# Kernel tuning notes

Measured on AMD Instinct MI355X. Metric: run time of the kernel, lower is better.

Reference implementation:

```python
import jax, jax.numpy as jnp
import numpy as np

N, E = 50000, 640000
DIN, DH, DOUT = 128, 256, 128


def _glorot(k, i, o):
    return jax.random.normal(k, (i, o), jnp.float32) / np.sqrt(i)


def setup_inputs() -> dict:
    key = jax.random.key(0)
    ks = jax.random.split(key, 12)
    return {
        "x": jax.random.normal(ks[0], (N, DIN), jnp.float32),
        "edge_index": jax.random.randint(ks[1], (2, E), 0, N, dtype=jnp.int32),
        # SAGEConv 1: in -> hidden (lin_l on aggregated w/ bias, lin_r on root)
        "W1l": _glorot(ks[2], DIN, DH), "b1l": jnp.zeros((DH,), jnp.float32), "W1r": _glorot(ks[3], DIN, DH),
        "g1": jnp.ones((DH,), jnp.float32), "be1": jnp.zeros((DH,), jnp.float32),
        # skip projection (in != hidden)
        "Wsk": _glorot(ks[4], DIN, DH), "bsk": jnp.zeros((DH,), jnp.float32),
        # SAGEConv 2: hidden -> hidden
        "W2l": _glorot(ks[5], DH, DH), "b2l": jnp.zeros((DH,), jnp.float32), "W2r": _glorot(ks[6], DH, DH),
        "g2": jnp.ones((DH,), jnp.float32), "be2": jnp.zeros((DH,), jnp.float32),
        # SAGEConv 3: hidden -> out
        "W3l": _glorot(ks[7], DH, DOUT), "b3l": jnp.zeros((DOUT,), jnp.float32), "W3r": _glorot(ks[8], DH, DOUT),
    }


def _sage_conv(x, src, dst, Wl, bl, Wr, n):
    # mean aggregation of source features into destination nodes
    msg = x[src]                                                 # [E, d]
    agg = jax.ops.segment_sum(msg, dst, num_segments=n)          # [N, d]
    cnt = jax.ops.segment_sum(jnp.ones((src.shape[0],), x.dtype), dst, num_segments=n)
    agg = agg / jnp.maximum(cnt, 1.0)[:, None]
    return agg @ Wl + bl + x @ Wr


def _layernorm(x, g, b):
    mu = jnp.mean(x, axis=-1, keepdims=True)
    var = jnp.mean((x - mu) ** 2, axis=-1, keepdims=True)
    return (x - mu) * jax.lax.rsqrt(var + 1e-5) * g + b


def reference(x, edge_index, W1l, b1l, W1r, g1, be1, Wsk, bsk,
              W2l, b2l, W2r, g2, be2, W3l, b3l, W3r):
    src, dst = edge_index[0], edge_index[1]
    n = x.shape[0]
    # layer 0: conv -> LN -> relu -> (dropout p=0, eval) -> skip via projection
    h = _sage_conv(x, src, dst, W1l, b1l, W1r, n)
    h = jax.nn.relu(_layernorm(h, g1, be1))
    h = h + (x @ Wsk + bsk)
    # layer 1: conv -> LN -> relu -> residual add (shapes match)
    h2 = _sage_conv(h, src, dst, W2l, b2l, W2r, n)
    h2 = jax.nn.relu(_layernorm(h2, g2, be2)) + h
    # final conv (no norm/act)
    return _sage_conv(h2, src, dst, W3l, b3l, W3r, n)
```

## Files before the change

### kernel.cpp

```cpp
#include <hip/hip_runtime.h>


typedef float floatx4 __attribute__((ext_vector_type(4)));
typedef float floatx2 __attribute__((ext_vector_type(2)));
typedef short bf16x8 __attribute__((ext_vector_type(8)));

__device__ inline unsigned short f2bf(float f) {
    unsigned u = __float_as_uint(f);
    unsigned r = (u + 0x7fffu + ((u >> 16) & 1u)) >> 16;
    return (unsigned short)r;
}
__device__ inline float bf2f_lo(unsigned v) { return __uint_as_float(v << 16); }
__device__ inline float bf2f_hi(unsigned v) { return __uint_as_float(v & 0xffff0000u); }

__device__ inline void gl_lds16(const void* g, void* l) {
    __builtin_amdgcn_global_load_lds((const __attribute__((address_space(1))) unsigned int*)g,
                                     (__attribute__((address_space(3))) unsigned int*)l,
                                     16, 0, 0);
}

__global__ void hist_kernel(const int* __restrict__ dst, int* __restrict__ cnt, int E) {
    int i = blockIdx.x * blockDim.x + threadIdx.x;
    if (i < E) atomicAdd(&cnt[dst[i]], 1);
}

#define SCAN_CHUNK 2048

__global__ __launch_bounds__(256) void scan_blocksums(const int* __restrict__ cnt,
                                                      int* __restrict__ bsum, int N) {
    __shared__ int sh[256];
    int t = threadIdx.x;
    int base = blockIdx.x * SCAN_CHUNK + t * 8;
    int s = 0;
#pragma unroll
    for (int i = 0; i < 8; i++) {
        int idx = base + i;
        if (idx < N) s += cnt[idx];
    }
    sh[t] = s;
    __syncthreads();
    for (int off = 1; off < 256; off <<= 1) {
        int v = (t >= off) ? sh[t - off] : 0;
        __syncthreads();
        sh[t] += v;
        __syncthreads();
    }
    if (t == 255) bsum[blockIdx.x] = sh[255];
}

__global__ __launch_bounds__(256) void scan_bsums(const int* __restrict__ bsum,
                                                  int* __restrict__ boff, int NB,
                                                  int* __restrict__ rowptr, int N, int E) {
    __shared__ int sh[256];
    int t = threadIdx.x;
    int v = (t < NB) ? bsum[t] : 0;
    sh[t] = v;
    __syncthreads();
    for (int off = 1; off < 256; off <<= 1) {
        int u = (t >= off) ? sh[t - off] : 0;
        __syncthreads();
        sh[t] += u;
        __syncthreads();
    }
    if (t < NB) boff[t] = sh[t] - v;
    if (t == 0) rowptr[N] = E;
}

__global__ __launch_bounds__(256) void scan_final(const int* __restrict__ cnt,
                                                  const int* __restrict__ boff,
                                                  int* __restrict__ rowptr,
                                                  int* __restrict__ cursor,
                                                  float* __restrict__ invdeg, int N) {
    __shared__ int sh[256];
    int t = threadIdx.x;
    int base = blockIdx.x * SCAN_CHUNK + t * 8;
    int c[8];
    int s = 0;
#pragma unroll
    for (int i = 0; i < 8; i++) {
        int idx = base + i;
        c[i] = (idx < N) ? cnt[idx] : 0;
        s += c[i];
    }
    sh[t] = s;
    __syncthreads();
    for (int off = 1; off < 256; off <<= 1) {
        int v = (t >= off) ? sh[t - off] : 0;
        __syncthreads();
        sh[t] += v;
        __syncthreads();
    }
    int run = boff[blockIdx.x] + sh[t] - s;
#pragma unroll
    for (int i = 0; i < 8; i++) {
        int idx = base + i;
        if (idx < N) {
            rowptr[idx] = run;
            cursor[idx] = run;
            invdeg[idx] = 1.0f / (float)(c[i] > 1 ? c[i] : 1);
            run += c[i];
        }
    }
}

__global__ void scatter_kernel(const int* __restrict__ src, const int* __restrict__ dst,
                               int* __restrict__ cursor, int* __restrict__ col, int E) {
    int i = blockIdx.x * blockDim.x + threadIdx.x;
    if (i < E) {
        int p = atomicAdd(&cursor[dst[i]], 1);
        col[p] = src[i];
    }
}

__global__ void prep_weights(const float* __restrict__ W1l, const float* __restrict__ W1r,
                             const float* __restrict__ Wsk, const float* __restrict__ W2l,
                             const float* __restrict__ W2r, const float* __restrict__ W3l,
                             const float* __restrict__ W3r, const float* __restrict__ b1l,
                             const float* __restrict__ bsk,
                             unsigned short* __restrict__ WtC, unsigned short* __restrict__ Wt2,
                             unsigned short* __restrict__ Wt3, float* __restrict__ biasC) {
    int i = blockIdx.x * blockDim.x + threadIdx.x;
    if (i < 32768) {
        int k = i >> 8, n = i & 255;
        WtC[n * 256 + k] = f2bf(W1l[i]);
    } else if (i < 65536) {
        int j = i - 32768, k = j >> 8, n = j & 255;
        WtC[n * 256 + 128 + k] = f2bf(W1r[j]);
    } else if (i < 98304) {
        int j = i - 65536, k = j >> 8, n = j & 255;
        WtC[(256 + n) * 256 + 128 + k] = f2bf(Wsk[j]);
    } else if (i < 131072) {
        int j = i - 98304, k = j >> 8, n = j & 255;
        WtC[(256 + n) * 256 + k] = 0;
    } else if (i < 196608) {
        int j = i - 131072, k = j >> 8, n = j & 255;
        Wt2[n * 512 + k] = f2bf(W2l[j]);
    } else if (i < 262144) {
        int j = i - 196608, k = j >> 8, n = j & 255;
        Wt2[n * 512 + 256 + k] = f2bf(W2r[j]);
    } else if (i < 294912) {
        int j = i - 262144, k = j >> 7, n = j & 127;
        Wt3[n * 256 + k] = f2bf(W3l[j]);
    } else if (i < 327680) {
        int j = i - 294912, k = j >> 7, n = j & 127;
        Wt3[(128 + n) * 256 + k] = f2bf(W3r[j]);
    } else if (i < 328192) {
        int j = i - 327680;
        biasC[j] = (j < 256) ? b1l[j] : bsk[j - 256];
    }
}

__global__ void cvt_x_kernel(const float* __restrict__ x, unsigned short* __restrict__ A1cat, int total) {
    int i = blockIdx.x * blockDim.x + threadIdx.x;
    if (i >= total) return;
    int r = i >> 7, c = i & 127;
    A1cat[(size_t)r * 256 + 128 + c] = f2bf(x[i]);
}

__global__ __launch_bounds__(256) void agg_bf16_v3(const int* __restrict__ rowptr,
                                                   const int* __restrict__ col,
                                                   const float* __restrict__ invdeg,
                                                   const unsigned short* __restrict__ X, int xstride,
                                                   unsigned short* __restrict__ out, int ostride, int N) {
    int wid = (blockIdx.x * blockDim.x + threadIdx.x) >> 6;
    int lane = threadIdx.x & 63;
    if (wid >= N) return;
    int half = lane >> 5;
    int sub = lane & 31;
    int off = blockIdx.y * 128 + sub * 4;
    const unsigned short* Xo = X + off;
    int s = rowptr[wid], e = rowptr[wid + 1];
    float a0 = 0.f, a1 = 0.f, a2 = 0.f, a3 = 0.f;
    for (int j = s + half; j < e; j += 8) {
        int j1 = (j + 2 < e) ? j + 2 : j;
        int j2 = (j + 4 < e) ? j + 4 : j;
        int j3 = (j + 6 < e) ? j + 6 : j;
        float m1 = (j + 2 < e) ? 1.f : 0.f;
        float m2 = (j + 4 < e) ? 1.f : 0.f;
        float m3 = (j + 6 < e) ? 1.f : 0.f;
        int c0 = col[j], c1 = col[j1], c2 = col[j2], c3 = col[j3];
        uint2 v0 = *(const uint2*)(Xo + (size_t)c0 * xstride);
        uint2 v1 = *(const uint2*)(Xo + (size_t)c1 * xstride);
        uint2 v2 = *(const uint2*)(Xo + (size_t)c2 * xstride);
        uint2 v3 = *(const uint2*)(Xo + (size_t)c3 * xstride);
        a0 += bf2f_lo(v0.x); a1 += bf2f_hi(v0.x); a2 += bf2f_lo(v0.y); a3 += bf2f_hi(v0.y);
        a0 = fmaf(m1, bf2f_lo(v1.x), a0); a1 = fmaf(m1, bf2f_hi(v1.x), a1);
        a2 = fmaf(m1, bf2f_lo(v1.y), a2); a3 = fmaf(m1, bf2f_hi(v1.y), a3);
        a0 = fmaf(m2, bf2f_lo(v2.x), a0); a1 = fmaf(m2, bf2f_hi(v2.x), a1);
        a2 = fmaf(m2, bf2f_lo(v2.y), a2); a3 = fmaf(m2, bf2f_hi(v2.y), a3);
        a0 = fmaf(m3, bf2f_lo(v3.x), a0); a1 = fmaf(m3, bf2f_hi(v3.x), a1);
        a2 = fmaf(m3, bf2f_lo(v3.y), a2); a3 = fmaf(m3, bf2f_hi(v3.y), a3);
    }
    a0 += __shfl_xor(a0, 32, 64);
    a1 += __shfl_xor(a1, 32, 64);
    a2 += __shfl_xor(a2, 32, 64);
    a3 += __shfl_xor(a3, 32, 64);
    if (half == 0) {
        float inv = invdeg[wid];
        ushort4 o;
        o.x = f2bf(a0 * inv); o.y = f2bf(a1 * inv);
        o.z = f2bf(a2 * inv); o.w = f2bf(a3 * inv);
        *(ushort4*)(out + (size_t)wid * ostride + off) = o;
    }
}

__device__ inline void accum_fp8(uint2 v, float m, float* a) {
    floatx2 p;
    p = __builtin_amdgcn_cvt_pk_f32_fp8(v.x, false); a[0] = fmaf(m, p.x, a[0]); a[1] = fmaf(m, p.y, a[1]);
    p = __builtin_amdgcn_cvt_pk_f32_fp8(v.x, true);  a[2] = fmaf(m, p.x, a[2]); a[3] = fmaf(m, p.y, a[3]);
    p = __builtin_amdgcn_cvt_pk_f32_fp8(v.y, false); a[4] = fmaf(m, p.x, a[4]); a[5] = fmaf(m, p.y, a[5]);
    p = __builtin_amdgcn_cvt_pk_f32_fp8(v.y, true);  a[6] = fmaf(m, p.x, a[6]); a[7] = fmaf(m, p.y, a[7]);
}

__global__ __launch_bounds__(256) void agg_fp8_256(const int* __restrict__ rowptr,
                                                   const int* __restrict__ col,
                                                   const float* __restrict__ invdeg,
                                                   const unsigned char* __restrict__ H8,
                                                   unsigned short* __restrict__ out, int ostride, int N) {
    int wid = (blockIdx.x * blockDim.x + threadIdx.x) >> 6;
    int lane = threadIdx.x & 63;
    if (wid >= N) return;
    int half = lane >> 5;
    int sub = lane & 31;
    const unsigned char* Ho = H8 + sub * 8;
    int s = rowptr[wid], e = rowptr[wid + 1];
    float a[8] = {0.f, 0.f, 0.f, 0.f, 0.f, 0.f, 0.f, 0.f};
    for (int j = s + half; j < e; j += 8) {
        int j1 = (j + 2 < e) ? j + 2 : j;
        int j2 = (j + 4 < e) ? j + 4 : j;
        int j3 = (j + 6 < e) ? j + 6 : j;
        float m1 = (j + 2 < e) ? 1.f : 0.f;
        float m2 = (j + 4 < e) ? 1.f : 0.f;
        float m3 = (j + 6 < e) ? 1.f : 0.f;
        int c0 = col[j], c1 = col[j1], c2 = col[j2], c3 = col[j3];
        uint2 v0 = *(const uint2*)(Ho + (size_t)c0 * 256);
        uint2 v1 = *(const uint2*)(Ho + (size_t)c1 * 256);
        uint2 v2 = *(const uint2*)(Ho + (size_t)c2 * 256);
        uint2 v3 = *(const uint2*)(Ho + (size_t)c3 * 256);
        accum_fp8(v0, 1.f, a);
        accum_fp8(v1, m1, a);
        accum_fp8(v2, m2, a);
        accum_fp8(v3, m3, a);
    }
#pragma unroll
    for (int i = 0; i < 8; i++) a[i] += __shfl_xor(a[i], 32, 64);
    if (half == 0) {
        float inv = invdeg[wid];
        uint4 o;
        o.x = (unsigned)f2bf(a[0] * inv) | ((unsigned)f2bf(a[1] * inv) << 16);
        o.y = (unsigned)f2bf(a[2] * inv) | ((unsigned)f2bf(a[3] * inv) << 16);
        o.z = (unsigned)f2bf(a[4] * inv) | ((unsigned)f2bf(a[5] * inv) << 16);
        o.w = (unsigned)f2bf(a[6] * inv) | ((unsigned)f2bf(a[7] * inv) << 16);
        *(uint4*)(out + (size_t)wid * ostride + sub * 8) = o;
    }
}

__global__ __launch_bounds__(256) void agg_final_v3(const int* __restrict__ rowptr,
                                                    const int* __restrict__ col,
                                                    const float* __restrict__ invdeg,
                                                    const unsigned short* __restrict__ T,
                                                    const float* __restrict__ R,
                                                    float* __restrict__ out, int N) {
    int wid = (blockIdx.x * blockDim.x + threadIdx.x) >> 6;
    int lane = threadIdx.x & 63;
    if (wid >= N) return;
    int half = lane >> 5;
    int sub = lane & 31;
    const unsigned short* To = T + sub * 4;
    int s = rowptr[wid], e = rowptr[wid + 1];
    float a0 = 0.f, a1 = 0.f, a2 = 0.f, a3 = 0.f;
    for (int j = s + half; j < e; j += 8) {
        int j1 = (j + 2 < e) ? j + 2 : j;
        int j2 = (j + 4 < e) ? j + 4 : j;
        int j3 = (j + 6 < e) ? j + 6 : j;
        float m1 = (j + 2 < e) ? 1.f : 0.f;
        float m2 = (j + 4 < e) ? 1.f : 0.f;
        float m3 = (j + 6 < e) ? 1.f : 0.f;
        int c0 = col[j], c1 = col[j1], c2 = col[j2], c3 = col[j3];
        uint2 v0 = *(const uint2*)(To + (size_t)c0 * 128);
        uint2 v1 = *(const uint2*)(To + (size_t)c1 * 128);
        uint2 v2 = *(const uint2*)(To + (size_t)c2 * 128);
        uint2 v3 = *(const uint2*)(To + (size_t)c3 * 128);
        a0 += bf2f_lo(v0.x); a1 += bf2f_hi(v0.x); a2 += bf2f_lo(v0.y); a3 += bf2f_hi(v0.y);
        a0 = fmaf(m1, bf2f_lo(v1.x), a0); a1 = fmaf(m1, bf2f_hi(v1.x), a1);
        a2 = fmaf(m1, bf2f_lo(v1.y), a2); a3 = fmaf(m1, bf2f_hi(v1.y), a3);
        a0 = fmaf(m2, bf2f_lo(v2.x), a0); a1 = fmaf(m2, bf2f_hi(v2.x), a1);
        a2 = fmaf(m2, bf2f_lo(v2.y), a2); a3 = fmaf(m2, bf2f_hi(v2.y), a3);
        a0 = fmaf(m3, bf2f_lo(v3.x), a0); a1 = fmaf(m3, bf2f_hi(v3.x), a1);
        a2 = fmaf(m3, bf2f_lo(v3.y), a2); a3 = fmaf(m3, bf2f_hi(v3.y), a3);
    }
    a0 += __shfl_xor(a0, 32, 64);
    a1 += __shfl_xor(a1, 32, 64);
    a2 += __shfl_xor(a2, 32, 64);
    a3 += __shfl_xor(a3, 32, 64);
    if (half == 0) {
        float inv = invdeg[wid];
        float4 r = *(const float4*)(R + (size_t)wid * 128 + sub * 4);
        float4 o;
        o.x = a0 * inv + r.x;
        o.y = a1 * inv + r.y;
        o.z = a2 * inv + r.z;
        o.w = a3 * inv + r.w;
        *(float4*)(out + (size_t)wid * 128 + sub * 4) = o;
    }
}

template <int KIT, int SPLIT>
__global__ __launch_bounds__(256) void gemm_lds(const unsigned short* __restrict__ A, int lda,
                                                const unsigned short* __restrict__ B, int ldb,
                                                const float* __restrict__ bias,
                                                unsigned short* __restrict__ C0, int ldc0,
                                                float* __restrict__ C1, int M) {
    __shared__ __align__(16) char smem[34816];
    unsigned short* sA = (unsigned short*)smem;
    unsigned short* sB = sA + 128 * 64;
    int t = threadIdx.x;
    int lane = t & 63, w = t >> 6;
    int bm = blockIdx.x * 128, bn = blockIdx.y * 128;
    int wm = (w >> 1) * 64, wn = (w & 1) * 64;
    int m16 = lane & 15, kq = lane >> 4;

    floatx4 acc[4][4];
#pragma unroll
    for (int i = 0; i < 4; i++)
#pragma unroll
        for (int j = 0; j < 4; j++) acc[i][j] = (floatx4){0.f, 0.f, 0.f, 0.f};

    const int c_row = t >> 3;
    const int kc = (t & 7) ^ (c_row & 7);
    const int srcOff = kc * 8;
    const int fsw = (m16 & 7);

    for (int kt = 0; kt < KIT; kt++) {
        int k0 = kt * 64;
#pragma unroll
        for (int i = 0; i < 4; i++) {
            int rowA = bm + i * 32 + c_row;
            if (rowA > M - 1) rowA = M - 1;
            gl_lds16(A + (size_t)rowA * lda + k0 + srcOff, (void*)&sA[(size_t)(i * 256 + t) * 8]);
            gl_lds16(B + (size_t)(bn + i * 32 + c_row) * ldb + k0 + srcOff,
                     (void*)&sB[(size_t)(i * 256 + t) * 8]);
        }
        __syncthreads();
#pragma unroll
        for (int ks = 0; ks < 2; ks++) {
            int kcl = (ks << 2) | kq;
            bf16x8 af[4], bfr[4];
#pragma unroll
            for (int mi = 0; mi < 4; mi++)
                af[mi] = *(const bf16x8*)&sA[(wm + mi * 16 + m16) * 64 + (kcl ^ fsw) * 8];
#pragma unroll
            for (int ni = 0; ni < 4; ni++)
                bfr[ni] = *(const bf16x8*)&sB[(wn + ni * 16 + m16) * 64 + (kcl ^ fsw) * 8];
#pragma unroll
            for (int mi = 0; mi < 4; mi++)
#pragma unroll
                for (int ni = 0; ni < 4; ni++)
                    acc[mi][ni] = __builtin_amdgcn_mfma_f32_16x16x32_bf16(af[mi], bfr[ni], acc[mi][ni], 0, 0, 0);
        }
        __syncthreads();
    }

    float* wb = (float*)smem + w * (64 * 34);
    const float* bias0 = (SPLIT == 0) ? bias : ((bn == 0) ? nullptr : bias);
#pragma unroll
    for (int h = 0; h < 2; h++) {
#pragma unroll
        for (int nj = 0; nj < 2; nj++) {
            int ni = h * 2 + nj;
#pragma unroll
            for (int mi = 0; mi < 4; mi++)
#pragma unroll
                for (int r = 0; r < 4; r++)
                    wb[(mi * 16 + kq * 4 + r) * 34 + nj * 16 + m16] = acc[mi][ni][r];
        }
        asm volatile("s_waitcnt lgkmcnt(0)" ::: "memory");
        if (SPLIT == 0 || bn == 0) {
            int rsub = lane >> 2, c8 = (lane & 3) * 8;
            int ldc = (SPLIT == 0) ? ldc0 : 128;
            int gcol = ((SPLIT == 0) ? bn : 0) + wn + h * 32 + c8;
            float bv[8];
#pragma unroll
            for (int j = 0; j < 8; j++) bv[j] = bias0 ? bias0[gcol + j] : 0.f;
#pragma unroll
            for (int it = 0; it < 4; it++) {
                int rr = it * 16 + rsub;
                int grow = bm + wm + rr;
                float v0 = wb[rr * 34 + c8 + 0] + bv[0];
                float v1 = wb[rr * 34 + c8 + 1] + bv[1];
                float v2 = wb[rr * 34 + c8 + 2] + bv[2];
                float v3 = wb[rr * 34 + c8 + 3] + bv[3];
                float v4 = wb[rr * 34 + c8 + 4] + bv[4];
                float v5 = wb[rr * 34 + c8 + 5] + bv[5];
                float v6 = wb[rr * 34 + c8 + 6] + bv[6];
                float v7 = wb[rr * 34 + c8 + 7] + bv[7];
                uint4 o;
                o.x = (unsigned)f2bf(v0) | ((unsigned)f2bf(v1) << 16);
                o.y = (unsigned)f2bf(v2) | ((unsigned)f2bf(v3) << 16);
                o.z = (unsigned)f2bf(v4) | ((unsigned)f2bf(v5) << 16);
                o.w = (unsigned)f2bf(v6) | ((unsigned)f2bf(v7) << 16);
                if (grow < M) *(uint4*)(C0 + (size_t)grow * ldc + gcol) = o;
            }
        } else {
            int rsub = lane >> 3, c4 = (lane & 7) * 4;
            int gcol = wn + h * 32 + c4;
            float bv[4];
#pragma unroll
            for (int j = 0; j < 4; j++) bv[j] = bias0[gcol + j];
#pragma unroll
            for (int it = 0; it < 8; it++) {
                int rr = it * 8 + rsub;
                int grow = bm + wm + rr;
                float4 o;
                o.x = wb[rr * 34 + c4 + 0] + bv[0];
                o.y = wb[rr * 34 + c4 + 1] + bv[1];
                o.z = wb[rr * 34 + c4 + 2] + bv[2];
                o.w = wb[rr * 34 + c4 + 3] + bv[3];
                if (grow < M) *(float4*)(C1 + (size_t)grow * 128 + gcol) = o;
            }
        }
        if (h == 0) asm volatile("s_waitcnt lgkmcnt(0)" ::: "memory");
    }
}

__global__ __launch_bounds__(256) void ln_fuse2(const unsigned short* __restrict__ u, int ustride,
                                                const unsigned short* __restrict__ a, int astride,
                                                const float* __restrict__ g, const float* __restrict__ b,
                                                unsigned short* __restrict__ out, int ostride,
                                                unsigned char* __restrict__ h8, int N) {
    int row = (blockIdx.x * blockDim.x + threadIdx.x) >> 6;
    int lane = threadIdx.x & 63;
    if (row >= N) return;
    uint2 uv = *(const uint2*)(u + (size_t)row * ustride + lane * 4);
    float v0 = bf2f_lo(uv.x), v1 = bf2f_hi(uv.x), v2 = bf2f_lo(uv.y), v3 = bf2f_hi(uv.y);
    float s = (v0 + v1) + (v2 + v3);
    float sq = (v0 * v0 + v1 * v1) + (v2 * v2 + v3 * v3);
    for (int off = 1; off < 64; off <<= 1) {
        s += __shfl_xor(s, off, 64);
        sq += __shfl_xor(sq, off, 64);
    }
    float mu = s * (1.f / 256.f);
    float var = sq * (1.f / 256.f) - mu * mu;
    float rs = rsqrtf(var + 1e-5f);
    float4 gv = *(const float4*)(g + lane * 4);
    float4 bv = *(const float4*)(b + lane * 4);
    uint2 av = *(const uint2*)(a + (size_t)row * astride + lane * 4);
    float a0 = bf2f_lo(av.x), a1 = bf2f_hi(av.x), a2 = bf2f_lo(av.y), a3 = bf2f_hi(av.y);
    float o0 = fmaxf((v0 - mu) * rs * gv.x + bv.x, 0.f) + a0;
    float o1 = fmaxf((v1 - mu) * rs * gv.y + bv.y, 0.f) + a1;
    float o2 = fmaxf((v2 - mu) * rs * gv.z + bv.z, 0.f) + a2;
    float o3 = fmaxf((v3 - mu) * rs * gv.w + bv.w, 0.f) + a3;
    ushort4 o;
    o.x = f2bf(o0); o.y = f2bf(o1); o.z = f2bf(o2); o.w = f2bf(o3);
    *(ushort4*)(out + (size_t)row * ostride + lane * 4) = o;
    if (h8) {
        unsigned wpk = 0;
        wpk = __builtin_amdgcn_cvt_pk_fp8_f32(o0, o1, wpk, false);
        wpk = __builtin_amdgcn_cvt_pk_fp8_f32(o2, o3, wpk, true);
        *(unsigned*)(h8 + (size_t)row * 256 + lane * 4) = wpk;
    }
}

extern "C" void kernel_launch(void* const* d_in, const int* in_sizes, int n_in,
                              void* d_out, int out_size, void* d_ws, size_t ws_size,
                              hipStream_t stream) {
    const float* x   = (const float*)d_in[0];
    const int*   ei  = (const int*)d_in[1];
    const float* W1l = (const float*)d_in[2];
    const float* b1l = (const float*)d_in[3];
    const float* W1r = (const float*)d_in[4];
    const float* g1  = (const float*)d_in[5];
    const float* be1 = (const float*)d_in[6];
    const float* Wsk = (const float*)d_in[7];
    const float* bsk = (const float*)d_in[8];
    const float* W2l = (const float*)d_in[9];
    const float* b2l = (const float*)d_in[10];
    const float* W2r = (const float*)d_in[11];
    const float* g2  = (const float*)d_in[12];
    const float* be2 = (const float*)d_in[13];
    const float* W3l = (const float*)d_in[14];
    const float* b3l = (const float*)d_in[15];
    const float* W3r = (const float*)d_in[16];

    const int N = in_sizes[0] / 128;
    const int E = in_sizes[1] / 2;
    const int* src = ei;
    const int* dst = ei + E;

    char* p = (char*)d_ws;
    auto alloc = [&](size_t bytes) {
        void* r = (void*)p;
        p += (bytes + 255) & ~(size_t)255;
        return r;
    };
    int*   cnt    = (int*)alloc(sizeof(int) * N);
    int*   rowptr = (int*)alloc(sizeof(int) * (N + 1));
    int*   cursor = (int*)alloc(sizeof(int) * N);
    float* invdeg = (float*)alloc(sizeof(float) * N);
    int*   col    = (int*)alloc(sizeof(int) * E);
    int*   bsum   = (int*)alloc(sizeof(int) * 256);
    int*   boff   = (int*)alloc(sizeof(int) * 256);
    unsigned short* A1cat = (unsigned short*)alloc(sizeof(short) * (size_t)N * 256);
    unsigned short* A2cat = (unsigned short*)alloc(sizeof(short) * (size_t)N * 512);
    unsigned short* U1    = (unsigned short*)alloc(sizeof(short) * (size_t)N * 512);
    float* r3 = (float*)alloc(sizeof(float) * (size_t)N * 128);
    unsigned char* H8 = (unsigned char*)alloc((size_t)N * 256);
    unsigned short* WtC = (unsigned short*)alloc(sizeof(short) * 512 * 256);
    unsigned short* Wt2 = (unsigned short*)alloc(sizeof(short) * 256 * 512);
    unsigned short* Wt3 = (unsigned short*)alloc(sizeof(short) * 256 * 256);
    float* biasC = (float*)alloc(sizeof(float) * 512);
    unsigned short* t3 = A1cat;
    unsigned short* u2 = U1;

    hipMemsetAsync(cnt, 0, sizeof(int) * N, stream);
    hist_kernel<<<(E + 255) / 256, 256, 0, stream>>>(dst, cnt, E);
    int NB = (N + SCAN_CHUNK - 1) / SCAN_CHUNK;
    scan_blocksums<<<NB, 256, 0, stream>>>(cnt, bsum, N);
    scan_bsums<<<1, 256, 0, stream>>>(bsum, boff, NB, rowptr, N, E);
    scan_final<<<NB, 256, 0, stream>>>(cnt, boff, rowptr, cursor, invdeg, N);
    scatter_kernel<<<(E + 255) / 256, 256, 0, stream>>>(src, dst, cursor, col, E);

    prep_weights<<<(328192 + 255) / 256, 256, 0, stream>>>(W1l, W1r, Wsk, W2l, W2r, W3l, W3r,
                                                           b1l, bsk, WtC, Wt2, Wt3, biasC);
    cvt_x_kernel<<<((N * 128) + 255) / 256, 256, 0, stream>>>(x, A1cat, N * 128);

    int aggBlocks = (N + 3) / 4;
    int mBlocks = (N + 127) / 128;

    agg_bf16_v3<<<dim3(aggBlocks, 1), 256, 0, stream>>>(rowptr, col, invdeg, A1cat + 128, 256, A1cat, 256, N);
    gemm_lds<4, 0><<<dim3(mBlocks, 4), 256, 0, stream>>>(A1cat, 256, WtC, 256, biasC, U1, 512, nullptr, N);
    ln_fuse2<<<aggBlocks, 256, 0, stream>>>(U1, 512, U1 + 256, 512, g1, be1, A2cat + 256, 512, H8, N);

    agg_fp8_256<<<aggBlocks, 256, 0, stream>>>(rowptr, col, invdeg, H8, A2cat, 512, N);
    gemm_lds<8, 0><<<dim3(mBlocks, 2), 256, 0, stream>>>(A2cat, 512, Wt2, 512, b2l, u2, 256, nullptr, N);
    ln_fuse2<<<aggBlocks, 256, 0, stream>>>(u2, 256, A2cat + 256, 512, g2, be2, A2cat, 512, nullptr, N);

    gemm_lds<4, 1><<<dim3(mBlocks, 2), 256, 0, stream>>>(A2cat, 512, Wt3, 256, b3l, t3, 128, r3, N);
    agg_final_v3<<<aggBlocks, 256, 0, stream>>>(rowptr, col, invdeg, t3, r3, (float*)d_out, N);
}
```

Baseline: 389.3 us.

## Widen GEMM N-tile to reuse A across two B panels; gather layer-1 input in fp8

The GEMM kernel now computes two 128-column B panels per block, so each A tile loaded into LDS is reused twice and the grid halves in N. The first-layer aggregation now gathers an fp8 copy of x, written by a vectorized conversion kernel alongside the bf16 copy, which halves the bytes read per edge. The costs are twice the accumulator registers (lower occupancy), more LDS per block, and lower aggregation precision for layer 1.

After: 376.8 us. 3.2% less time.

```diff
diff --git a/kernel.cpp b/kernel.cpp
--- a/kernel.cpp
+++ b/kernel.cpp
@@ -150,58 +150,19 @@
     }
 }
 
-__global__ void cvt_x_kernel(const float* __restrict__ x, unsigned short* __restrict__ A1cat, int total) {
+__global__ void cvt_x2(const float* __restrict__ x, unsigned short* __restrict__ A1cat,
+                       unsigned char* __restrict__ X8, int total32) {
     int i = blockIdx.x * blockDim.x + threadIdx.x;
-    if (i >= total) return;
-    int r = i >> 7, c = i & 127;
-    A1cat[(size_t)r * 256 + 128 + c] = f2bf(x[i]);
-}
-
-__global__ __launch_bounds__(256) void agg_bf16_v3(const int* __restrict__ rowptr,
-                                                   const int* __restrict__ col,
-                                                   const float* __restrict__ invdeg,
-                                                   const unsigned short* __restrict__ X, int xstride,
-                                                   unsigned short* __restrict__ out, int ostride, int N) {
-    int wid = (blockIdx.x * blockDim.x + threadIdx.x) >> 6;
-    int lane = threadIdx.x & 63;
-    if (wid >= N) return;
-    int half = lane >> 5;
-    int sub = lane & 31;
-    int off = blockIdx.y * 128 + sub * 4;
-    const unsigned short* Xo = X + off;
-    int s = rowptr[wid], e = rowptr[wid + 1];
-    float a0 = 0.f, a1 = 0.f, a2 = 0.f, a3 = 0.f;
-    for (int j = s + half; j < e; j += 8) {
-        int j1 = (j + 2 < e) ? j + 2 : j;
-        int j2 = (j + 4 < e) ? j + 4 : j;
-        int j3 = (j + 6 < e) ? j + 6 : j;
-        float m1 = (j + 2 < e) ? 1.f : 0.f;
-        float m2 = (j + 4 < e) ? 1.f : 0.f;
-        float m3 = (j + 6 < e) ? 1.f : 0.f;
-        int c0 = col[j], c1 = col[j1], c2 = col[j2], c3 = col[j3];
-        uint2 v0 = *(const uint2*)(Xo + (size_t)c0 * xstride);
-        uint2 v1 = *(const uint2*)(Xo + (size_t)c1 * xstride);
-        uint2 v2 = *(const uint2*)(Xo + (size_t)c2 * xstride);
-        uint2 v3 = *(const uint2*)(Xo + (size_t)c3 * xstride);
-        a0 += bf2f_lo(v0.x); a1 += bf2f_hi(v0.x); a2 += bf2f_lo(v0.y); a3 += bf2f_hi(v0.y);
-        a0 = fmaf(m1, bf2f_lo(v1.x), a0); a1 = fmaf(m1, bf2f_hi(v1.x), a1);
-        a2 = fmaf(m1, bf2f_lo(v1.y), a2); a3 = fmaf(m1, bf2f_hi(v1.y), a3);
-        a0 = fmaf(m2, bf2f_lo(v2.x), a0); a1 = fmaf(m2, bf2f_hi(v2.x), a1);
-        a2 = fmaf(m2, bf2f_lo(v2.y), a2); a3 = fmaf(m2, bf2f_hi(v2.y), a3);
-        a0 = fmaf(m3, bf2f_lo(v3.x), a0); a1 = fmaf(m3, bf2f_hi(v3.x), a1);
-        a2 = fmaf(m3, bf2f_lo(v3.y), a2); a3 = fmaf(m3, bf2f_hi(v3.y), a3);
-    }
-    a0 += __shfl_xor(a0, 32, 64);
-    a1 += __shfl_xor(a1, 32, 64);
-    a2 += __shfl_xor(a2, 32, 64);
-    a3 += __shfl_xor(a3, 32, 64);
-    if (half == 0) {
-        float inv = invdeg[wid];
-        ushort4 o;
-        o.x = f2bf(a0 * inv); o.y = f2bf(a1 * inv);
-        o.z = f2bf(a2 * inv); o.w = f2bf(a3 * inv);
-        *(ushort4*)(out + (size_t)wid * ostride + off) = o;
-    }
+    if (i >= total32) return;
+    int r = i >> 5, c4 = (i & 31) * 4;
+    float4 v = *(const float4*)(x + (size_t)r * 128 + c4);
+    ushort4 o;
+    o.x = f2bf(v.x); o.y = f2bf(v.y); o.z = f2bf(v.z); o.w = f2bf(v.w);
+    *(ushort4*)(A1cat + (size_t)r * 256 + 128 + c4) = o;
+    unsigned wpk = 0;
+    wpk = __builtin_amdgcn_cvt_pk_fp8_f32(v.x, v.y, wpk, false);
+    wpk = __builtin_amdgcn_cvt_pk_fp8_f32(v.z, v.w, wpk, true);
+    *(unsigned*)(X8 + (size_t)r * 128 + c4) = wpk;
 }
 
 __device__ inline void accum_fp8(uint2 v, float m, float* a) {
@@ -210,6 +171,52 @@
     p = __builtin_amdgcn_cvt_pk_f32_fp8(v.x, true);  a[2] = fmaf(m, p.x, a[2]); a[3] = fmaf(m, p.y, a[3]);
     p = __builtin_amdgcn_cvt_pk_f32_fp8(v.y, false); a[4] = fmaf(m, p.x, a[4]); a[5] = fmaf(m, p.y, a[5]);
     p = __builtin_amdgcn_cvt_pk_f32_fp8(v.y, true);  a[6] = fmaf(m, p.x, a[6]); a[7] = fmaf(m, p.y, a[7]);
+}
+
+__global__ __launch_bounds__(256) void agg_fp8_128(const int* __restrict__ rowptr,
+                                                   const int* __restrict__ col,
+                                                   const float* __restrict__ invdeg,
+                                                   const unsigned char* __restrict__ X8,
+                                                   unsigned short* __restrict__ out, int ostride, int N) {
+    int wid = (blockIdx.x * blockDim.x + threadIdx.x) >> 6;
+    int lane = threadIdx.x & 63;
+    if (wid >= N) return;
+    int q = lane >> 4;
+    int sub = lane & 15;
+    const unsigned char* Xo = X8 + sub * 8;
+    int s = rowptr[wid], e = rowptr[wid + 1];
+    float a[8] = {0.f, 0.f, 0.f, 0.f, 0.f, 0.f, 0.f, 0.f};
+    for (int j = s + q; j < e; j += 16) {
+        int j1 = (j + 4 < e) ? j + 4 : j;
+        int j2 = (j + 8 < e) ? j + 8 : j;
+        int j3 = (j + 12 < e) ? j + 12 : j;
+        float m1 = (j + 4 < e) ? 1.f : 0.f;
+        float m2 = (j + 8 < e) ? 1.f : 0.f;
+        float m3 = (j + 12 < e) ? 1.f : 0.f;
+        int c0 = col[j], c1 = col[j1], c2 = col[j2], c3 = col[j3];
+        uint2 v0 = *(const uint2*)(Xo + (size_t)c0 * 128);
+        uint2 v1 = *(const uint2*)(Xo + (size_t)c1 * 128);
+        uint2 v2 = *(const uint2*)(Xo + (size_t)c2 * 128);
+        uint2 v3 = *(const uint2*)(Xo + (size_t)c3 * 128);
+        accum_fp8(v0, 1.f, a);
+        accum_fp8(v1, m1, a);
+        accum_fp8(v2, m2, a);
+        accum_fp8(v3, m3, a);
+    }
+#pragma unroll
+    for (int i = 0; i < 8; i++) {
+        a[i] += __shfl_xor(a[i], 16, 64);
+        a[i] += __shfl_xor(a[i], 32, 64);
+    }
+    if (q == 0) {
+        float inv = invdeg[wid];
+        uint4 o;
+        o.x = (unsigned)f2bf(a[0] * inv) | ((unsigned)f2bf(a[1] * inv) << 16);
+        o.y = (unsigned)f2bf(a[2] * inv) | ((unsigned)f2bf(a[3] * inv) << 16);
+        o.z = (unsigned)f2bf(a[4] * inv) | ((unsigned)f2bf(a[5] * inv) << 16);
+        o.w = (unsigned)f2bf(a[6] * inv) | ((unsigned)f2bf(a[7] * inv) << 16);
+        *(uint4*)(out + (size_t)wid * ostride + sub * 8) = o;
+    }
 }
 
 __global__ __launch_bounds__(256) void agg_fp8_256(const int* __restrict__ rowptr,
@@ -305,26 +312,30 @@
     }
 }
 
-template <int KIT, int SPLIT>
-__global__ __launch_bounds__(256) void gemm_lds(const unsigned short* __restrict__ A, int lda,
-                                                const unsigned short* __restrict__ B, int ldb,
-                                                const float* __restrict__ bias,
-                                                unsigned short* __restrict__ C0, int ldc0,
-                                                float* __restrict__ C1, int M) {
-    __shared__ __align__(16) char smem[34816];
+template <int KIT, int NP, int SPLIT>
+__global__ __launch_bounds__(256) void gemm_lds2(const unsigned short* __restrict__ A, int lda,
+                                                 const unsigned short* __restrict__ B, int ldb,
+                                                 const float* __restrict__ bias,
+                                                 unsigned short* __restrict__ C0, int ldc0,
+                                                 float* __restrict__ C1, int M) {
+    constexpr int STAGE = 128 * 64 * 2;
+    constexpr int SMEM_SZ = (STAGE * (1 + NP) > 34816) ? STAGE * (1 + NP) : 34816;
+    __shared__ __align__(16) char smem[SMEM_SZ];
     unsigned short* sA = (unsigned short*)smem;
-    unsigned short* sB = sA + 128 * 64;
     int t = threadIdx.x;
     int lane = t & 63, w = t >> 6;
-    int bm = blockIdx.x * 128, bn = blockIdx.y * 128;
+    int bm = blockIdx.x * 128;
+    int bn0 = blockIdx.y * 128 * NP;
     int wm = (w >> 1) * 64, wn = (w & 1) * 64;
     int m16 = lane & 15, kq = lane >> 4;
 
-    floatx4 acc[4][4];
-#pragma unroll
-    for (int i = 0; i < 4; i++)
-#pragma unroll
-        for (int j = 0; j < 4; j++) acc[i][j] = (floatx4){0.f, 0.f, 0.f, 0.f};
+    floatx4 acc[NP][4][4];
+#pragma unroll
+    for (int p = 0; p < NP; p++)
+#pragma unroll
+        for (int i = 0; i < 4; i++)
+#pragma unroll
+            for (int j = 0; j < 4; j++) acc[p][i][j] = (floatx4){0.f, 0.f, 0.f, 0.f};
 
     const int c_row = t >> 3;
     const int kc = (t & 7) ^ (c_row & 7);
@@ -338,88 +349,101 @@
             int rowA = bm + i * 32 + c_row;
             if (rowA > M - 1) rowA = M - 1;
             gl_lds16(A + (size_t)rowA * lda + k0 + srcOff, (void*)&sA[(size_t)(i * 256 + t) * 8]);
-            gl_lds16(B + (size_t)(bn + i * 32 + c_row) * ldb + k0 + srcOff,
-                     (void*)&sB[(size_t)(i * 256 + t) * 8]);
+#pragma unroll
+            for (int p = 0; p < NP; p++)
+                gl_lds16(B + (size_t)(bn0 + p * 128 + i * 32 + c_row) * ldb + k0 + srcOff,
+                         (void*)&sA[(size_t)((p + 1) * 128 * 64) + (size_t)(i * 256 + t) * 8]);
         }
         __syncthreads();
 #pragma unroll
         for (int ks = 0; ks < 2; ks++) {
             int kcl = (ks << 2) | kq;
-            bf16x8 af[4], bfr[4];
+            bf16x8 af[4];
 #pragma unroll
             for (int mi = 0; mi < 4; mi++)
                 af[mi] = *(const bf16x8*)&sA[(wm + mi * 16 + m16) * 64 + (kcl ^ fsw) * 8];
 #pragma unroll
-            for (int ni = 0; ni < 4; ni++)
-                bfr[ni] = *(const bf16x8*)&sB[(wn + ni * 16 + m16) * 64 + (kcl ^ fsw) * 8];
-#pragma unroll
-            for (int mi = 0; mi < 4; mi++)
+            for (int p = 0; p < NP; p++) {
+                const unsigned short* sB = sA + (p + 1) * 128 * 64;
+                bf16x8 bfr[4];
 #pragma unroll
                 for (int ni = 0; ni < 4; ni++)
-                    acc[mi][ni] = __builtin_amdgcn_mfma_f32_16x16x32_bf16(af[mi], bfr[ni], acc[mi][ni], 0, 0, 0);
-        }
-        __syncthreads();
-    }
-
-    float* wb = (float*)smem + w * (64 * 34);
-    const float* bias0 = (SPLIT == 0) ? bias : ((bn == 0) ? nullptr : bias);
-#pragma unroll
-    for (int h = 0; h < 2; h++) {
-#pragma unroll
-        for (int nj = 0; nj < 2; nj++) {
-            int ni = h * 2 + nj;
-#pragma unroll
-            for (int mi = 0; mi < 4; mi++)
-#pragma unroll
-                for (int r = 0; r < 4; r++)
-                    wb[(mi * 16 + kq * 4 + r) * 34 + nj * 16 + m16] = acc[mi][ni][r];
-        }
-        asm volatile("s_waitcnt lgkmcnt(0)" ::: "memory");
-        if (SPLIT == 0 || bn == 0) {
-            int rsub = lane >> 2, c8 = (lane & 3) * 8;
-            int ldc = (SPLIT == 0) ? ldc0 : 128;
-            int gcol = ((SPLIT == 0) ? bn : 0) + wn + h * 32 + c8;
-            float bv[8];
-#pragma unroll
-            for (int j = 0; j < 8; j++) bv[j] = bias0 ? bias0[gcol + j] : 0.f;
-#pragma unroll
-            for (int it = 0; it < 4; it++) {
-                int rr = it * 16 + rsub;
-                int grow = bm + wm + rr;
-                float v0 = wb[rr * 34 + c8 + 0] + bv[0];
-                float v1 = wb[rr * 34 + c8 + 1] + bv[1];
-                float v2 = wb[rr * 34 + c8 + 2] + bv[2];
-                float v3 = wb[rr * 34 + c8 + 3] + bv[3];
-                float v4 = wb[rr * 34 + c8 + 4] + bv[4];
-                float v5 = wb[rr * 34 + c8 + 5] + bv[5];
-                float v6 = wb[rr * 34 + c8 + 6] + bv[6];
-                float v7 = wb[rr * 34 + c8 + 7] + bv[7];
-                uint4 o;
-                o.x = (unsigned)f2bf(v0) | ((unsigned)f2bf(v1) << 16);
-                o.y = (unsigned)f2bf(v2) | ((unsigned)f2bf(v3) << 16);
-                o.z = (unsigned)f2bf(v4) | ((unsigned)f2bf(v5) << 16);
-                o.w = (unsigned)f2bf(v6) | ((unsigned)f2bf(v7) << 16);
-                if (grow < M) *(uint4*)(C0 + (size_t)grow * ldc + gcol) = o;
-            }
-        } else {
-            int rsub = lane >> 3, c4 = (lane & 7) * 4;
-            int gcol = wn + h * 32 + c4;
-            float bv[4];
-#pragma unroll
-            for (int j = 0; j < 4; j++) bv[j] = bias0[gcol + j];
-#pragma unroll
-            for (int it = 0; it < 8; it++) {
-                int rr = it * 8 + rsub;
-                int grow = bm + wm + rr;
-                float4 o;
-                o.x = wb[rr * 34 + c4 + 0] + bv[0];
-                o.y = wb[rr * 34 + c4 + 1] + bv[1];
-                o.z = wb[rr * 34 + c4 + 2] + bv[2];
-                o.w = wb[rr * 34 + c4 + 3] + bv[3];
-                if (grow < M) *(float4*)(C1 + (size_t)grow * 128 + gcol) = o;
+                    bfr[ni] = *(const bf16x8*)&sB[(wn + ni * 16 + m16) * 64 + (kcl ^ fsw) * 8];
+#pragma unroll
+                for (int mi = 0; mi < 4; mi++)
+#pragma unroll
+                    for (int ni = 0; ni < 4; ni++)
+                        acc[p][mi][ni] =
+                            __builtin_amdgcn_mfma_f32_16x16x32_bf16(af[mi], bfr[ni], acc[p][mi][ni], 0, 0, 0);
             }
         }
-        if (h == 0) asm volatile("s_waitcnt lgkmcnt(0)" ::: "memory");
+        __syncthreads();
+    }
+
+    float* wb = (float*)smem + w * (64 * 34);
+#pragma unroll
+    for (int p = 0; p < NP; p++) {
+        const bool isF32 = (SPLIT == 1 && p == 1);
+        const float* bp = (SPLIT == 0) ? (bias + bn0 + p * 128) : ((p == 0) ? nullptr : bias);
+#pragma unroll
+        for (int h = 0; h < 2; h++) {
+#pragma unroll
+            for (int nj = 0; nj < 2; nj++) {
+                int ni = h * 2 + nj;
+#pragma unroll
+                for (int mi = 0; mi < 4; mi++)
+#pragma unroll
+                    for (int r = 0; r < 4; r++)
+                        wb[(mi * 16 + kq * 4 + r) * 34 + nj * 16 + m16] = acc[p][mi][ni][r];
+            }
+            asm volatile("s_waitcnt lgkmcnt(0)" ::: "memory");
+            if (!isF32) {
+                int rsub = lane >> 2, c8 = (lane & 3) * 8;
+                int ldc = (SPLIT == 0) ? ldc0 : 128;
+                int lcol = wn + h * 32 + c8;
+                int colbase = ((SPLIT == 0) ? bn0 + p * 128 : 0) + lcol;
+                float bv[8];
+#pragma unroll
+                for (int j = 0; j < 8; j++) bv[j] = bp ? bp[lcol + j] : 0.f;
+#pragma unroll
+                for (int it = 0; it < 4; it++) {
+                    int rr = it * 16 + rsub;
+                    int grow = bm + wm + rr;
+                    float v0 = wb[rr * 34 + c8 + 0] + bv[0];
+                    float v1 = wb[rr * 34 + c8 + 1] + bv[1];
+                    float v2 = wb[rr * 34 + c8 + 2] + bv[2];
+                    float v3 = wb[rr * 34 + c8 + 3] + bv[3];
+                    float v4 = wb[rr * 34 + c8 + 4] + bv[4];
+                    float v5 = wb[rr * 34 + c8 + 5] + bv[5];
+                    float v6 = wb[rr * 34 + c8 + 6] + bv[6];
+                    float v7 = wb[rr * 34 + c8 + 7] + bv[7];
+                    uint4 o;
+                    o.x = (unsigned)f2bf(v0) | ((unsigned)f2bf(v1) << 16);
+                    o.y = (unsigned)f2bf(v2) | ((unsigned)f2bf(v3) << 16);
+                    o.z = (unsigned)f2bf(v4) | ((unsigned)f2bf(v5) << 16);
+                    o.w = (unsigned)f2bf(v6) | ((unsigned)f2bf(v7) << 16);
+                    if (grow < M) *(uint4*)(C0 + (size_t)grow * ldc + colbase) = o;
+                }
+            } else {
+                int rsub = lane >> 3, c4 = (lane & 7) * 4;
+                int gcol = wn + h * 32 + c4;
+                float bv[4];
+#pragma unroll
+                for (int j = 0; j < 4; j++) bv[j] = bp[gcol + j];
+#pragma unroll
+                for (int it = 0; it < 8; it++) {
+                    int rr = it * 8 + rsub;
+                    int grow = bm + wm + rr;
+                    float4 o;
+                    o.x = wb[rr * 34 + c4 + 0] + bv[0];
+                    o.y = wb[rr * 34 + c4 + 1] + bv[1];
+                    o.z = wb[rr * 34 + c4 + 2] + bv[2];
+                    o.w = wb[rr * 34 + c4 + 3] + bv[3];
+                    if (grow < M) *(float4*)(C1 + (size_t)grow * 128 + gcol) = o;
+                }
+            }
+            asm volatile("s_waitcnt lgkmcnt(0)" ::: "memory");
+        }
     }
 }
 
@@ -505,6 +529,7 @@
     unsigned short* U1    = (unsigned short*)alloc(sizeof(short) * (size_t)N * 512);
     float* r3 = (float*)alloc(sizeof(float) * (size_t)N * 128);
     unsigned char* H8 = (unsigned char*)alloc((size_t)N * 256);
+    unsigned char* X8 = (unsigned char*)alloc((size_t)N * 128);
     unsigned short* WtC = (unsigned short*)alloc(sizeof(short) * 512 * 256);
     unsigned short* Wt2 = (unsigned short*)alloc(sizeof(short) * 256 * 512);
     unsigned short* Wt3 = (unsigned short*)alloc(sizeof(short) * 256 * 256);
@@ -522,19 +547,19 @@
 
     prep_weights<<<(328192 + 255) / 256, 256, 0, stream>>>(W1l, W1r, Wsk, W2l, W2r, W3l, W3r,
                                                            b1l, bsk, WtC, Wt2, Wt3, biasC);
-    cvt_x_kernel<<<((N * 128) + 255) / 256, 256, 0, stream>>>(x, A1cat, N * 128);
+    cvt_x2<<<((N * 32) + 255) / 256, 256, 0, stream>>>(x, A1cat, X8, N * 32);
 
     int aggBlocks = (N + 3) / 4;
     int mBlocks = (N + 127) / 128;
 
-    agg_bf16_v3<<<dim3(aggBlocks, 1), 256, 0, stream>>>(rowptr, col, invdeg, A1cat + 128, 256, A1cat, 256, N);
-    gemm_lds<4, 0><<<dim3(mBlocks, 4), 256, 0, stream>>>(A1cat, 256, WtC, 256, biasC, U1, 512, nullptr, N);
+    agg_fp8_128<<<aggBlocks, 256, 0, stream>>>(rowptr, col, invdeg, X8, A1cat, 256, N);
+    gemm_lds2<4, 2, 0><<<dim3(mBlocks, 2), 256, 0, stream>>>(A1cat, 256, WtC, 256, biasC, U1, 512, nullptr, N);
     ln_fuse2<<<aggBlocks, 256, 0, stream>>>(U1, 512, U1 + 256, 512, g1, be1, A2cat + 256, 512, H8, N);
 
     agg_fp8_256<<<aggBlocks, 256, 0, stream>>>(rowptr, col, invdeg, H8, A2cat, 512, N);
-    gemm_lds<8, 0><<<dim3(mBlocks, 2), 256, 0, stream>>>(A2cat, 512, Wt2, 512, b2l, u2, 256, nullptr, N);
+    gemm_lds2<8, 2, 0><<<dim3(mBlocks, 1), 256, 0, stream>>>(A2cat, 512, Wt2, 512, b2l, u2, 256, nullptr, N);
     ln_fuse2<<<aggBlocks, 256, 0, stream>>>(u2, 256, A2cat + 256, 512, g2, be2, A2cat, 512, nullptr, N);
 
-    gemm_lds<4, 1><<<dim3(mBlocks, 2), 256, 0, stream>>>(A2cat, 512, Wt3, 256, b3l, t3, 128, r3, N);
+    gemm_lds2<4, 2, 1><<<dim3(mBlocks, 1), 256, 0, stream>>>(A2cat, 512, Wt3, 256, b3l, t3, 128, r3, N);
     agg_final_v3<<<aggBlocks, 256, 0, stream>>>(rowptr, col, invdeg, t3, r3, (float*)d_out, N);
 }
```
